# Performance work log

Measured on AMD Instinct MI355X. Metric: run time of the kernel, lower is better.

The kernel has to match this reference:

```python
import jax, jax.numpy as jnp
import numpy as np

N = 65536
E = 1048576
IN_DIM = 128
POS_DIM = 128  # num_nodes (ROI one-hot dim)
HID = 128


def _mk_params(key):
    # layer 0: local in = IN_DIM + POS_DIM; layer 1: local in = HID + POS_DIM
    dims = [(IN_DIM + POS_DIM, HID), (HID + POS_DIM, HID)]
    params = {}
    for l, (din, _) in enumerate(dims):
        ks = jax.random.split(jax.random.fold_in(key, l), 4)
        params[f"l{l}_lw1"] = jax.random.normal(ks[0], (din, HID), jnp.float32) * (1.0 / np.sqrt(din))
        params[f"l{l}_lb1"] = jnp.zeros((HID,), jnp.float32)
        params[f"l{l}_lw2"] = jax.random.normal(ks[1], (HID, HID), jnp.float32) * (1.0 / np.sqrt(HID))
        params[f"l{l}_lb2"] = jnp.zeros((HID,), jnp.float32)
        params[f"l{l}_gw1"] = jax.random.normal(ks[2], (HID, HID), jnp.float32) * (1.0 / np.sqrt(HID))
        params[f"l{l}_gb1"] = jnp.zeros((HID,), jnp.float32)
        params[f"l{l}_gw2"] = jax.random.normal(ks[3], (HID, HID), jnp.float32) * (1.0 / np.sqrt(HID))
        params[f"l{l}_gb2"] = jnp.zeros((HID,), jnp.float32)
    return params


def setup_inputs() -> dict:
    key = jax.random.key(0)
    k1, k2, k3, k4 = jax.random.split(key, 4)
    inp = {
        "x": jax.random.normal(k1, (N, IN_DIM), jnp.float32),
        "pos": jax.random.normal(k2, (N, POS_DIM), jnp.float32),
        "edge_index": jax.random.randint(k3, (2, E), 0, N, jnp.int64),
    }
    inp.update(_mk_params(k4))
    return inp


def _pointnet_conv(x, pos, src, dst, lw1, lb1, lw2, lb2, gw1, gb1, gw2, gb2):
    # message: concat(x_j, pos_j - pos_i) per edge -> local_nn (Lin-ReLU-Lin)
    msg = jnp.concatenate([x[src], pos[src] - pos[dst]], axis=1)  # [E', in+pos]
    h = jax.nn.relu(msg @ lw1 + lb1) @ lw2 + lb2                  # [E', HID]
    agg = jax.ops.segment_max(h, dst, num_segments=N)             # max aggr (PointNetConv default)
    return jax.nn.relu(agg @ gw1 + gb1) @ gw2 + gb2               # global_nn


def reference(x, pos, edge_index,
              l0_lw1, l0_lb1, l0_lw2, l0_lb2, l0_gw1, l0_gb1, l0_gw2, l0_gb2,
              l1_lw1, l1_lb1, l1_lw2, l1_lb2, l1_gw1, l1_gb1, l1_gw2, l1_gb2):
    # add_self_loops=True (PointNetConv default); ensures every node has an incoming edge
    loops = jnp.arange(N, dtype=edge_index.dtype)
    src = jnp.concatenate([edge_index[0], loops])
    dst = jnp.concatenate([edge_index[1], loops])
    h = _pointnet_conv(x, pos, src, dst, l0_lw1, l0_lb1, l0_lw2, l0_lb2,
                       l0_gw1, l0_gb1, l0_gw2, l0_gb2)
    h = _pointnet_conv(h, pos, src, dst, l1_lw1, l1_lb1, l1_lw2, l1_lb2,
                       l1_gw1, l1_gb1, l1_gw2, l1_gb2)
    return h
```

## Files before the change

### kernel.cpp

```cpp
#include <hip/hip_runtime.h>
#include <hip/hip_bf16.h>
#include <stdint.h>

#define NN 65536
#define NE 1048576
#define E2 (NE + NN)
#define HID 128
#define LP 136
#define RMAX 13
#define TP 129
#define TABW 1680
#define ENC_NEG 0x007FFFFFu

typedef _Float16 h8v __attribute__((ext_vector_type(8)));
typedef __fp16 fp16x2 __attribute__((ext_vector_type(2)));
typedef __attribute__((ext_vector_type(4))) float f32x4;

__device__ __forceinline__ uint32_t pkh(float a, float b){
    union { fp16x2 h; uint32_t u; } v;
    v.h = __builtin_amdgcn_cvt_pkrtz(a, b);
    return v.u;
}
__device__ __forceinline__ uint32_t encf(float x){
    union { float f; uint32_t u; } v; v.f = x;
    return v.u ^ (uint32_t)(((int32_t)v.u >> 31) | 0x80000000);
}
__device__ __forceinline__ float decf(uint32_t u){
    union { uint32_t u; float f; } v;
    v.u = u ^ (uint32_t)(~((int32_t)u >> 31) | 0x80000000);
    return v.f;
}

__device__ __forceinline__ void gl_lds16(const _Float16* g, _Float16* l){
    __builtin_amdgcn_global_load_lds(
        (const __attribute__((address_space(1))) uint32_t*)g,
        (__attribute__((address_space(3))) uint32_t*)l, 16, 0, 0);
}

__device__ __forceinline__ void dma_w(const _Float16* __restrict__ wT, _Float16* Ws,
                                      int wv, int lane){
    #pragma unroll
    for (int rnd = 0; rnd < 8; rnd++){
        int g = rnd*256 + wv*64 + lane;
        int r = g >> 4, kc = g & 15;
        gl_lds16(wT + r*HID + ((kc ^ (r & 15)) << 3),
                 Ws + rnd*2048 + wv*512);
    }
}
__device__ __forceinline__ void dma_w8(const _Float16* __restrict__ wT, _Float16* Ws,
                                       int wv, int lane){
    #pragma unroll
    for (int rnd = 0; rnd < 4; rnd++){
        int g = rnd*512 + wv*64 + lane;
        int r = g >> 4, kc = g & 15;
        gl_lds16(wT + r*HID + ((kc ^ (r & 15)) << 3),
                 Ws + rnd*4096 + wv*512);
    }
}

__device__ __forceinline__ void gemm_w(const _Float16* Ts, const _Float16* Ws,
                                       f32x4 (&acc)[8], int wv, int lq, int quad){
    #pragma unroll
    for (int k0 = 0; k0 < 128; k0 += 32){
        h8v af = *(const h8v*)(Ts + (wv*16 + lq)*LP + k0 + quad*8);
        const int kcb = k0 >> 3;
        #pragma unroll
        for (int ct = 0; ct < 8; ct++){
            h8v b = *(const h8v*)(Ws + (ct*16 + lq)*128 + (((kcb + quad) ^ lq) << 3));
            acc[ct] = __builtin_amdgcn_mfma_f32_16x16x32_f16(af, b, acc[ct], 0, 0, 0);
        }
    }
}

__device__ __forceinline__ void zero_acc8(f32x4 (&acc)[8]){
    #pragma unroll
    for (int b = 0; b < 8; b++) acc[b] = (f32x4){0.f, 0.f, 0.f, 0.f};
}

__device__ __forceinline__ void zero_acc(f32x4 (&acc)[2][8]){
    #pragma unroll
    for (int a = 0; a < 2; a++)
        #pragma unroll
        for (int b = 0; b < 8; b++)
            acc[a][b] = (f32x4){0.f, 0.f, 0.f, 0.f};
}

struct WT { const float* s[10]; _Float16* d[10]; };
__global__ void k_prep(WT w, uint32_t* cnt,
                       const float* lb2_0, const float* gw1_0, const float* gb1_0,
                       const float* lb2_1, const float* gw1_1, const float* gb1_1,
                       float* c1p){
    int b = blockIdx.x;
    int t = threadIdx.x;
    if (b < 10){
        __shared__ _Float16 T[128*136];
        const float* src = w.s[b];
        _Float16* dst = w.d[b];
        #pragma unroll
        for (int c = 0; c < 8; c++){
            int e8 = c*256 + t;
            int k = e8 >> 4, n0 = (e8 & 15) * 8;
            float4 f0 = *(const float4*)(src + k*128 + n0);
            float4 f1 = *(const float4*)(src + k*128 + n0 + 4);
            T[(n0+0)*136 + k] = (_Float16)f0.x;
            T[(n0+1)*136 + k] = (_Float16)f0.y;
            T[(n0+2)*136 + k] = (_Float16)f0.z;
            T[(n0+3)*136 + k] = (_Float16)f0.w;
            T[(n0+4)*136 + k] = (_Float16)f1.x;
            T[(n0+5)*136 + k] = (_Float16)f1.y;
            T[(n0+6)*136 + k] = (_Float16)f1.z;
            T[(n0+7)*136 + k] = (_Float16)f1.w;
        }
        __syncthreads();
        #pragma unroll
        for (int c = 0; c < 8; c++){
            int e8 = c*256 + t;
            int n = e8 >> 4, k0 = (e8 & 15) * 8;
            *(uint4*)(dst + n*128 + k0) = *(const uint4*)(&T[n*136 + k0]);
        }
    } else if (b < 266){
        cnt[(b - 10)*256 + t] = 1u;
    } else {
        int l = b - 266;
        int j = t;
        if (j < 128){
            const float* lb2 = l ? lb2_1 : lb2_0;
            const float* gw1 = l ? gw1_1 : gw1_0;
            float s = (l ? gb1_1 : gb1_0)[j];
            for (int k = 0; k < 128; k++) s += lb2[k] * gw1[k*128 + j];
            c1p[l*128 + j] = s;
        }
    }
}

__launch_bounds__(512, 4)
__global__ void k_histab3(const int* __restrict__ ei, uint32_t* __restrict__ cnt,
                          const float* __restrict__ x, const float* __restrict__ pos,
                          const _Float16* __restrict__ w1aT0, const _Float16* __restrict__ w1bT0,
                          const _Float16* __restrict__ w1bT1, const float* __restrict__ lb1_0,
                          _Float16* __restrict__ Ah, _Float16* __restrict__ Bh0,
                          _Float16* __restrict__ Bh1, uint32_t* __restrict__ agg){
    __shared__ _Float16 Ts[128*LP];
    __shared__ _Float16 Ws[128*128];
    __shared__ float b1s[128];
    const int tid = threadIdx.x;

    if (blockIdx.x >= 512){
        int e = (blockIdx.x - 512) * 512 + tid;
        atomicAdd(&cnt[ei[NE + e]], 1u);
        return;
    }

    const int node0 = blockIdx.x * 128;
    const int wv = tid >> 6, lane = tid & 63, lq = lane & 15, quad = lane >> 4;
    if (tid < 128) b1s[tid] = lb1_0[tid];

    {
        uint4* ap = (uint4*)(agg + (size_t)node0 * HID);
        uint4 v = make_uint4(ENC_NEG, ENC_NEG, ENC_NEG, ENC_NEG);
        #pragma unroll
        for (int i = 0; i < 8; i++) ap[tid + i*512] = v;
    }
    #pragma unroll
    for (int i = 0; i < 4; i++){
        int chunk = tid + i*512;
        int row = chunk >> 4, qc = chunk & 15;
        const float4* src = (const float4*)(pos + (size_t)(node0 + row)*HID + qc*8);
        float4 f0 = src[0], f1 = src[1];
        uint4 o; o.x = pkh(f0.x, f0.y); o.y = pkh(f0.z, f0.w);
        o.z = pkh(f1.x, f1.y); o.w = pkh(f1.z, f1.w);
        *(uint4*)(Ts + row*LP + qc*8) = o;
    }
    dma_w8(w1bT1, Ws, wv, lane);
    __syncthreads();

    f32x4 acc[8];
    zero_acc8(acc);
    gemm_w(Ts, Ws, acc, wv, lq, quad);
    __syncthreads();
    dma_w8(w1bT0, Ws, wv, lane);
    #pragma unroll
    for (int ct = 0; ct < 8; ct++)
        #pragma unroll
        for (int rg = 0; rg < 4; rg++)
            Bh1[(size_t)(node0 + wv*16 + quad*4 + rg)*HID + ct*16 + lq]
                = (_Float16)acc[ct][rg];
    __syncthreads();

    zero_acc8(acc);
    gemm_w(Ts, Ws, acc, wv, lq, quad);
    __syncthreads();

    #pragma unroll
    for (int i = 0; i < 4; i++){
        int chunk = tid + i*512;
        int row = chunk >> 4, qc = chunk & 15;
        const float4* src = (const float4*)(x + (size_t)(node0 + row)*HID + qc*8);
        float4 f0 = src[0], f1 = src[1];
        uint4 o; o.x = pkh(f0.x, f0.y); o.y = pkh(f0.z, f0.w);
        o.z = pkh(f1.x, f1.y); o.w = pkh(f1.z, f1.w);
        *(uint4*)(Ts + row*LP + qc*8) = o;
    }
    dma_w8(w1aT0, Ws, wv, lane);
    #pragma unroll
    for (int ct = 0; ct < 8; ct++)
        #pragma unroll
        for (int rg = 0; rg < 4; rg++)
            Bh0[(size_t)(node0 + wv*16 + quad*4 + rg)*HID + ct*16 + lq]
                = (_Float16)acc[ct][rg];
    __syncthreads();

    gemm_w(Ts, Ws, acc, wv, lq, quad);

    #pragma unroll
    for (int ct = 0; ct < 8; ct++)
        #pragma unroll
        for (int rg = 0; rg < 4; rg++){
            int c = ct*16 + lq;
            Ah[(size_t)(node0 + wv*16 + quad*4 + rg)*HID + c]
                = (_Float16)(acc[ct][rg] + b1s[c]);
        }
}

__global__ void k_scan1(const uint32_t* __restrict__ cnt, uint32_t* __restrict__ bsum){
    __shared__ uint32_t ps[256];
    int t = threadIdx.x;
    ps[t] = cnt[blockIdx.x*256 + t]; __syncthreads();
    for (int off = 128; off > 0; off >>= 1){
        if (t < off) ps[t] += ps[t + off];
        __syncthreads();
    }
    if (t == 0) bsum[blockIdx.x] = ps[0];
}
__global__ void k_scan23(const uint32_t* __restrict__ cnt, const uint32_t* __restrict__ bsum,
                         uint32_t* __restrict__ cur){
    __shared__ uint32_t ps[256];
    __shared__ uint32_t bs[256];
    int t = threadIdx.x, b = blockIdx.x, i = b*256 + t;
    uint32_t bb = bsum[b];
    bs[t] = bsum[t];
    uint32_t v = cnt[i];
    ps[t] = v; __syncthreads();
    for (int off = 1; off < 256; off <<= 1){
        uint32_t u = (t >= off) ? ps[t - off] : 0u;
        uint32_t w = (t >= off) ? bs[t - off] : 0u;
        __syncthreads();
        ps[t] += u; bs[t] += w;
        __syncthreads();
    }
    cur[i] = (bs[b] - bb) + ps[t] - v;
}
__global__ void k_scatter(const int* __restrict__ ei, uint32_t* cur,
                          uint2* __restrict__ sedge){
    int e = blockIdx.x * 256 + threadIdx.x;
    if (e >= E2) return;
    uint32_t s, d;
    if (e < NE){ s = (uint32_t)ei[e]; d = (uint32_t)ei[NE + e]; }
    else { s = d = (uint32_t)(e - NE); }
    uint32_t p = atomicAdd(&cur[d], 1u);
    sedge[p] = make_uint2(s, d);
}

__launch_bounds__(256, 4)
__global__ void k_edge(const uint2* __restrict__ sedge,
                       const _Float16* __restrict__ Ah, const _Float16* __restrict__ Bh,
                       const _Float16* __restrict__ w2T,
                       uint32_t* __restrict__ agg){
    __shared__ _Float16 Ws[128*128];
    __shared__ __align__(16) uint32_t tab[TABW];
    __shared__ int ds_s[128];
    __shared__ unsigned long long masks_s[2];
    __shared__ int run_dst_s[RMAX];
    const int tid = threadIdx.x;
    const int bid = blockIdx.x;
    const int lb  = (bid & 7) * (E2/128/8) + (bid >> 3);
    const int e0 = lb * 128;
    const int wv = tid >> 6, lane = tid & 63, lq = lane & 15, quad = lane >> 4;
    const int r0 = wv*32 + lq, r1 = r0 + 16;

    const uint2 ea = sedge[e0 + r0];
    const uint2 eb = sedge[e0 + r1];
    int d_cur = 0;
    if (tid < 128) d_cur = (int)sedge[e0 + tid].y;

    dma_w(w2T, Ws, wv, lane);

    const _Float16* a0p = Ah + (size_t)ea.x*HID + quad*8;
    const _Float16* a1p = Ah + (size_t)eb.x*HID + quad*8;
    const _Float16* b0p = Bh + (size_t)ea.y*HID + quad*8;
    const _Float16* b1p = Bh + (size_t)eb.y*HID + quad*8;
    h8v A0[4], A1[4], B0[4], B1[4];
    #pragma unroll
    for (int i = 0; i < 4; i++){
        A0[i] = *(const h8v*)(a0p + 32*i);
        A1[i] = *(const h8v*)(a1p + 32*i);
        B0[i] = *(const h8v*)(b0p + 32*i);
        B1[i] = *(const h8v*)(b1p + 32*i);
    }

    bool flag = false;
    if (tid < 128){
        ds_s[tid] = d_cur;
        int d_up  = __shfl_up(d_cur, 1);
        int d_b63 = __shfl((int)eb.y, 15);
        if (tid & 63) flag = (d_cur != d_up);
        else          flag = (tid == 0) ? true : (d_cur != d_b63);
        unsigned long long m = __ballot(flag);
        if ((tid & 63) == 0) masks_s[tid >> 6] = m;
    }
    {
        uint4* t4 = (uint4*)tab;
        const uint4 vneg = make_uint4(ENC_NEG, ENC_NEG, ENC_NEG, ENC_NEG);
        #pragma unroll
        for (int i = 0; i < 2; i++){
            int idx = tid + i*256;
            if (idx < TABW/4) t4[idx] = vneg;
        }
    }
    __syncthreads();

    const unsigned long long m0 = masks_s[0], m1 = masks_s[1];
    const int c0 = __popcll(m0);
    const int nruns = c0 + __popcll(m1);

    if (flag){
        int r;
        if (tid < 64) r = __popcll(m0 & ((2ull << tid) - 1)) - 1;
        else          r = c0 + __popcll(m1 & ((2ull << (tid-64)) - 1)) - 1;
        if (r < RMAX) run_dst_s[r] = d_cur;
    }

    f32x4 acc[2][8];
    zero_acc(acc);

    const h8v zero8 = (h8v)(_Float16)0;
    __builtin_amdgcn_s_setprio(1);
    #pragma unroll
    for (int i = 0; i < 4; i++){
        h8v a0 = __builtin_elementwise_max(A0[i] - B0[i], zero8);
        h8v a1 = __builtin_elementwise_max(A1[i] - B1[i], zero8);
        const int kcb = i*4;
        #pragma unroll
        for (int ct = 0; ct < 8; ct++){
            h8v b = *(const h8v*)(Ws + (ct*16 + lq)*128 + (((kcb + quad) ^ lq) << 3));
            acc[0][ct] = __builtin_amdgcn_mfma_f32_16x16x32_f16(a0, b, acc[0][ct], 0, 0, 0);
            acc[1][ct] = __builtin_amdgcn_mfma_f32_16x16x32_f16(a1, b, acc[1][ct], 0, 0, 0);
        }
    }
    __builtin_amdgcn_s_setprio(0);

    #pragma unroll
    for (int rt = 0; rt < 2; rt++){
        const int rb = wv*32 + rt*16 + quad*4;
        int rid[4];
        #pragma unroll
        for (int i = 0; i < 4; i++){
            int r = rb + i;
            if (r < 64) rid[i] = __popcll(m0 & ((2ull << r) - 1)) - 1;
            else        rid[i] = c0 + __popcll(m1 & ((2ull << (r-64)) - 1)) - 1;
        }
        const bool b01 = rid[1] != rid[0];
        const bool b12 = rid[2] != rid[1];
        const bool b23 = rid[3] != rid[2];
        #pragma unroll
        for (int ct = 0; ct < 8; ct++){
            const int c = ct*16 + lq;
            float v0 = acc[rt][ct][0], v1 = acc[rt][ct][1];
            float v2 = acc[rt][ct][2], v3 = acc[rt][ct][3];
            #define FLUSH(ID, R, V) do{ uint32_t ev = encf(V); \
                if (__builtin_expect((ID) < RMAX, 1)) atomicMax(&tab[(ID)*TP + c], ev); \
                else atomicMax(&agg[(size_t)ds_s[R]*HID + c], ev); }while(0)
            if (b01) FLUSH(rid[0], rb+0, v0); else v1 = fmaxf(v1, v0);
            if (b12) FLUSH(rid[1], rb+1, v1); else v2 = fmaxf(v2, v1);
            if (b23) FLUSH(rid[2], rb+2, v2); else v3 = fmaxf(v3, v2);
            FLUSH(rid[3], rb+3, v3);
            #undef FLUSH
        }
    }
    __syncthreads();

    {
        const int c = tid & 127;
        const int ntab = nruns < RMAX ? nruns : RMAX;
        for (int r = tid >> 7; r < ntab; r += 2){
            uint32_t v = tab[r*TP + c];
            uint32_t* dst = &agg[(size_t)run_dst_s[r]*HID + c];
            if (r == 0 || r == nruns-1 || nruns > RMAX) atomicMax(dst, v);
            else *dst = v;
        }
    }
}

__launch_bounds__(512, 4)
__global__ void k_gnn_ab(uint32_t* __restrict__ agg,
                         const _Float16* __restrict__ g1T, const _Float16* __restrict__ g2T,
                         const float* __restrict__ c1p, const float* __restrict__ gb2,
                         const _Float16* __restrict__ w1aT1, const _Float16* __restrict__ Bh1,
                         const float* __restrict__ lb1_1,
                         _Float16* __restrict__ Ah){
    __shared__ _Float16 Ts[128*LP];
    __shared__ _Float16 Ws[128*128];
    __shared__ float c1s[128];
    __shared__ float c2s[128];
    __shared__ float b1s[128];
    const int tid = threadIdx.x;
    const int node0 = blockIdx.x * 128;
    const int wv = tid >> 6, lane = tid & 63, lq = lane & 15, quad = lane >> 4;
    if (tid < 128){ c1s[tid] = c1p[tid]; c2s[tid] = gb2[tid]; b1s[tid] = lb1_1[tid]; }

    {
        const uint4 vneg = make_uint4(ENC_NEG, ENC_NEG, ENC_NEG, ENC_NEG);
        #pragma unroll
        for (int i = 0; i < 8; i++){
            int chunk = tid + i*512;
            int row = chunk >> 5, qc = chunk & 31;
            uint4* ga = (uint4*)(agg + (size_t)(node0 + row)*HID + qc*4);
            uint4 u = *ga; *ga = vneg;
            uint2 o; o.x = pkh(decf(u.x), decf(u.y)); o.y = pkh(decf(u.z), decf(u.w));
            *(uint2*)(Ts + row*LP + qc*4) = o;
        }
    }
    dma_w8(g1T, Ws, wv, lane);
    __syncthreads();

    f32x4 acc[8];
    zero_acc8(acc);
    gemm_w(Ts, Ws, acc, wv, lq, quad);
    __syncthreads();
    dma_w8(g2T, Ws, wv, lane);
    #pragma unroll
    for (int ct = 0; ct < 8; ct++)
        #pragma unroll
        for (int rg = 0; rg < 4; rg++){
            int c = ct*16 + lq;
            Ts[(wv*16 + quad*4 + rg)*LP + c] = (_Float16)fmaxf(acc[ct][rg] + c1s[c], 0.f);
        }
    __syncthreads();

    zero_acc8(acc);
    gemm_w(Ts, Ws, acc, wv, lq, quad);
    __syncthreads();
    dma_w8(w1aT1, Ws, wv, lane);
    #pragma unroll
    for (int ct = 0; ct < 8; ct++)
        #pragma unroll
        for (int rg = 0; rg < 4; rg++){
            int c = ct*16 + lq;
            Ts[(wv*16 + quad*4 + rg)*LP + c] = (_Float16)(acc[ct][rg] + c2s[c]);
        }
    __syncthreads();

    _Float16 bres[8][4];
    #pragma unroll
    for (int ct = 0; ct < 8; ct++)
        #pragma unroll
        for (int rg = 0; rg < 4; rg++)
            bres[ct][rg] = Bh1[(size_t)(node0 + wv*16 + quad*4 + rg)*HID + ct*16 + lq];

    zero_acc8(acc);
    gemm_w(Ts, Ws, acc, wv, lq, quad);

    #pragma unroll
    for (int ct = 0; ct < 8; ct++)
        #pragma unroll
        for (int rg = 0; rg < 4; rg++){
            int c = ct*16 + lq;
            float v = acc[ct][rg] + (float)bres[ct][rg] + b1s[c];
            Ah[(size_t)(node0 + wv*16 + quad*4 + rg)*HID + c] = (_Float16)v;
        }
}

__launch_bounds__(512, 4)
__global__ void k_gnn(const uint32_t* __restrict__ agg,
                      const _Float16* __restrict__ g1T, const _Float16* __restrict__ g2T,
                      const float* __restrict__ c1p, const float* __restrict__ gb2,
                      float* __restrict__ outf){
    __shared__ _Float16 Ts[128*LP];
    __shared__ _Float16 Ws[128*128];
    __shared__ float c1s[128];
    __shared__ float c2s[128];
    const int tid = threadIdx.x;
    const int node0 = blockIdx.x * 128;
    const int wv = tid >> 6, lane = tid & 63, lq = lane & 15, quad = lane >> 4;
    if (tid < 128){ c1s[tid] = c1p[tid]; c2s[tid] = gb2[tid]; }

    {
        #pragma unroll
        for (int i = 0; i < 8; i++){
            int chunk = tid + i*512;
            int row = chunk >> 5, qc = chunk & 31;
            const uint4* ga = (const uint4*)(agg + (size_t)(node0 + row)*HID + qc*4);
            uint4 u = *ga;
            uint2 o; o.x = pkh(decf(u.x), decf(u.y)); o.y = pkh(decf(u.z), decf(u.w));
            *(uint2*)(Ts + row*LP + qc*4) = o;
        }
    }
    dma_w8(g1T, Ws, wv, lane);
    __syncthreads();

    f32x4 acc[8];
    zero_acc8(acc);
    gemm_w(Ts, Ws, acc, wv, lq, quad);
    __syncthreads();
    dma_w8(g2T, Ws, wv, lane);
    #pragma unroll
    for (int ct = 0; ct < 8; ct++)
        #pragma unroll
        for (int rg = 0; rg < 4; rg++){
            int c = ct*16 + lq;
            Ts[(wv*16 + quad*4 + rg)*LP + c] = (_Float16)fmaxf(acc[ct][rg] + c1s[c], 0.f);
        }
    __syncthreads();

    zero_acc8(acc);
    gemm_w(Ts, Ws, acc, wv, lq, quad);

    #pragma unroll
    for (int ct = 0; ct < 8; ct++)
        #pragma unroll
        for (int rg = 0; rg < 4; rg++){
            int c = ct*16 + lq;
            outf[(size_t)(node0 + wv*16 + quad*4 + rg)*HID + c] = acc[ct][rg] + c2s[c];
        }
}

extern "C" void kernel_launch(void* const* d_in, const int* in_sizes, int n_in,
                              void* d_out, int out_size, void* d_ws, size_t ws_size,
                              hipStream_t stream){
    const float* x   = (const float*)d_in[0];
    const float* pos = (const float*)d_in[1];
    const int*   ei  = (const int*)d_in[2];
    const float* W[16];
    for (int i = 0; i < 16; i++) W[i] = (const float*)d_in[3 + i];

    uint8_t* p = (uint8_t*)d_ws;
    _Float16* wT[10];
    for (int i = 0; i < 10; i++) wT[i] = (_Float16*)(p + (size_t)i * 32768);
    size_t off = 10 * 32768;
    _Float16* Ah  = (_Float16*)(p + off); off += (size_t)NN * HID * 2;
    _Float16* Bh0 = (_Float16*)(p + off); off += (size_t)NN * HID * 2;
    _Float16* Bh1 = (_Float16*)(p + off); off += (size_t)NN * HID * 2;
    uint32_t* agg = (uint32_t*)(p + off); off += (size_t)NN * HID * 4;
    uint32_t* cnt = (uint32_t*)(p + off); off += (size_t)NN * 4;
    uint32_t* cur = (uint32_t*)(p + off); off += (size_t)NN * 4;
    uint32_t* bsum = (uint32_t*)(p + off); off += 256 * 4;
    uint32_t* bofs = (uint32_t*)(p + off); off += 256 * 4;
    float* c1p = (float*)(p + off); off += 256 * 4;
    uint2* sedge = (uint2*)(p + off); off += (size_t)E2 * 8;
    (void)ws_size; (void)in_sizes; (void)n_in; (void)out_size; (void)bofs;

    WT wt;
    for (int l = 0; l < 2; l++){
        wt.s[5*l + 0] = W[8*l + 0];
        wt.s[5*l + 1] = W[8*l + 0] + 128*128;
        wt.s[5*l + 2] = W[8*l + 2];
        wt.s[5*l + 3] = W[8*l + 4];
        wt.s[5*l + 4] = W[8*l + 6];
        for (int j = 0; j < 5; j++) wt.d[5*l + j] = wT[5*l + j];
    }
    k_prep<<<268, 256, 0, stream>>>(wt, cnt, W[3], W[4], W[5], W[11], W[12], W[13], c1p);

    k_histab3<<<512 + NE/512, 512, 0, stream>>>(ei, cnt, x, pos, wT[0], wT[1], wT[6],
                                                W[1], Ah, Bh0, Bh1, agg);
    k_scan1<<<256, 256, 0, stream>>>(cnt, bsum);
    k_scan23<<<256, 256, 0, stream>>>(cnt, bsum, cur);
    k_scatter<<<(E2 + 255)/256, 256, 0, stream>>>(ei, cur, sedge);

    k_edge<<<E2/128, 256, 0, stream>>>(sedge, Ah, Bh0, wT[2], agg);
    k_gnn_ab<<<NN/128, 512, 0, stream>>>(agg, wT[3], wT[4], c1p, W[7],
                                         wT[5], Bh1, W[9], Ah);
    k_edge<<<E2/128, 256, 0, stream>>>(sedge, Ah, Bh1, wT[7], agg);
    k_gnn<<<NN/128, 512, 0, stream>>>(agg, wT[8], wT[9], c1p + 128, W[15],
                                      (float*)d_out);
}
```

Measured before the change: 453.2 us.

## Reuse histogram atomic ranks in scatter and pack edges into 16-bit pairs

The destination-count histogram now stores each edge's atomicAdd return value as a rank. The scatter kernel then computes each edge's sorted position as cur[d] + rank with no second round of atomics. Sorted edges are packed as one 32-bit word holding two 16-bit node ids, which halves the edge-list traffic in the scatter and in both edge-kernel passes. The s_setprio hints around the MFMA loop are also removed. In exchange it adds a rank buffer of NE words and relies on node ids fitting in 16 bits.

New measurement: 411.2 us. 1.1x faster.

```diff
diff --git a/kernel.cpp b/kernel.cpp
--- a/kernel.cpp
+++ b/kernel.cpp
@@ -135,6 +135,7 @@
 
 __launch_bounds__(512, 4)
 __global__ void k_histab3(const int* __restrict__ ei, uint32_t* __restrict__ cnt,
+                          uint32_t* __restrict__ rank,
                           const float* __restrict__ x, const float* __restrict__ pos,
                           const _Float16* __restrict__ w1aT0, const _Float16* __restrict__ w1bT0,
                           const _Float16* __restrict__ w1bT1, const float* __restrict__ lb1_0,
@@ -147,7 +148,7 @@
 
     if (blockIdx.x >= 512){
         int e = (blockIdx.x - 512) * 512 + tid;
-        atomicAdd(&cnt[ei[NE + e]], 1u);
+        rank[e] = atomicAdd(&cnt[ei[NE + e]], 1u);
         return;
     }
 
@@ -250,19 +251,26 @@
     }
     cur[i] = (bs[b] - bb) + ps[t] - v;
 }
-__global__ void k_scatter(const int* __restrict__ ei, uint32_t* cur,
-                          uint2* __restrict__ sedge){
-    int e = blockIdx.x * 256 + threadIdx.x;
-    if (e >= E2) return;
-    uint32_t s, d;
-    if (e < NE){ s = (uint32_t)ei[e]; d = (uint32_t)ei[NE + e]; }
-    else { s = d = (uint32_t)(e - NE); }
-    uint32_t p = atomicAdd(&cur[d], 1u);
-    sedge[p] = make_uint2(s, d);
+
+__global__ void k_scatter(const int* __restrict__ ei, const uint32_t* __restrict__ cur,
+                          const uint32_t* __restrict__ rank,
+                          uint32_t* __restrict__ sedge){
+    int e = blockIdx.x * 512 + threadIdx.x;
+    uint32_t p, v;
+    if (e < NE){
+        uint32_t s = (uint32_t)ei[e], d = (uint32_t)ei[NE + e];
+        p = cur[d] + rank[e];
+        v = s | (d << 16);
+    } else {
+        uint32_t d = (uint32_t)(e - NE);
+        p = cur[d];
+        v = d | (d << 16);
+    }
+    sedge[p] = v;
 }
 
 __launch_bounds__(256, 4)
-__global__ void k_edge(const uint2* __restrict__ sedge,
+__global__ void k_edge(const uint32_t* __restrict__ sedge,
                        const _Float16* __restrict__ Ah, const _Float16* __restrict__ Bh,
                        const _Float16* __restrict__ w2T,
                        uint32_t* __restrict__ agg){
@@ -278,17 +286,17 @@
     const int wv = tid >> 6, lane = tid & 63, lq = lane & 15, quad = lane >> 4;
     const int r0 = wv*32 + lq, r1 = r0 + 16;
 
-    const uint2 ea = sedge[e0 + r0];
-    const uint2 eb = sedge[e0 + r1];
+    const uint32_t ea = sedge[e0 + r0];
+    const uint32_t eb = sedge[e0 + r1];
     int d_cur = 0;
-    if (tid < 128) d_cur = (int)sedge[e0 + tid].y;
+    if (tid < 128) d_cur = (int)(sedge[e0 + tid] >> 16);
 
     dma_w(w2T, Ws, wv, lane);
 
-    const _Float16* a0p = Ah + (size_t)ea.x*HID + quad*8;
-    const _Float16* a1p = Ah + (size_t)eb.x*HID + quad*8;
-    const _Float16* b0p = Bh + (size_t)ea.y*HID + quad*8;
-    const _Float16* b1p = Bh + (size_t)eb.y*HID + quad*8;
+    const _Float16* a0p = Ah + (size_t)(ea & 0xFFFFu)*HID + quad*8;
+    const _Float16* a1p = Ah + (size_t)(eb & 0xFFFFu)*HID + quad*8;
+    const _Float16* b0p = Bh + (size_t)(ea >> 16)*HID + quad*8;
+    const _Float16* b1p = Bh + (size_t)(eb >> 16)*HID + quad*8;
     h8v A0[4], A1[4], B0[4], B1[4];
     #pragma unroll
     for (int i = 0; i < 4; i++){
@@ -302,7 +310,7 @@
     if (tid < 128){
         ds_s[tid] = d_cur;
         int d_up  = __shfl_up(d_cur, 1);
-        int d_b63 = __shfl((int)eb.y, 15);
+        int d_b63 = __shfl((int)(eb >> 16), 15);
         if (tid & 63) flag = (d_cur != d_up);
         else          flag = (tid == 0) ? true : (d_cur != d_b63);
         unsigned long long m = __ballot(flag);
@@ -334,7 +342,6 @@
     zero_acc(acc);
 
     const h8v zero8 = (h8v)(_Float16)0;
-    __builtin_amdgcn_s_setprio(1);
     #pragma unroll
     for (int i = 0; i < 4; i++){
         h8v a0 = __builtin_elementwise_max(A0[i] - B0[i], zero8);
@@ -347,7 +354,6 @@
             acc[1][ct] = __builtin_amdgcn_mfma_f32_16x16x32_f16(a1, b, acc[1][ct], 0, 0, 0);
         }
     }
-    __builtin_amdgcn_s_setprio(0);
 
     #pragma unroll
     for (int rt = 0; rt < 2; rt++){
@@ -544,10 +550,10 @@
     uint32_t* cnt = (uint32_t*)(p + off); off += (size_t)NN * 4;
     uint32_t* cur = (uint32_t*)(p + off); off += (size_t)NN * 4;
     uint32_t* bsum = (uint32_t*)(p + off); off += 256 * 4;
-    uint32_t* bofs = (uint32_t*)(p + off); off += 256 * 4;
     float* c1p = (float*)(p + off); off += 256 * 4;
-    uint2* sedge = (uint2*)(p + off); off += (size_t)E2 * 8;
-    (void)ws_size; (void)in_sizes; (void)n_in; (void)out_size; (void)bofs;
+    uint32_t* rank = (uint32_t*)(p + off); off += (size_t)NE * 4;
+    uint32_t* sedge = (uint32_t*)(p + off); off += (size_t)E2 * 4;
+    (void)ws_size; (void)in_sizes; (void)n_in; (void)out_size;
 
     WT wt;
     for (int l = 0; l < 2; l++){
@@ -560,11 +566,12 @@
     }
     k_prep<<<268, 256, 0, stream>>>(wt, cnt, W[3], W[4], W[5], W[11], W[12], W[13], c1p);
 
-    k_histab3<<<512 + NE/512, 512, 0, stream>>>(ei, cnt, x, pos, wT[0], wT[1], wT[6],
-                                                W[1], Ah, Bh0, Bh1, agg);
+    k_histab3<<<512 + NE/512, 512, 0, stream>>>(ei, cnt, rank, x, pos,
+                                                wT[0], wT[1], wT[6], W[1],
+                                                Ah, Bh0, Bh1, agg);
     k_scan1<<<256, 256, 0, stream>>>(cnt, bsum);
     k_scan23<<<256, 256, 0, stream>>>(cnt, bsum, cur);
-    k_scatter<<<(E2 + 255)/256, 256, 0, stream>>>(ei, cur, sedge);
+    k_scatter<<<E2/512, 512, 0, stream>>>(ei, cur, rank, sedge);
 
     k_edge<<<E2/128, 256, 0, stream>>>(sedge, Ah, Bh0, wT[2], agg);
     k_gnn_ab<<<NN/128, 512, 0, stream>>>(agg, wT[3], wT[4], c1p, W[7],
```
